# Optimization experiments

Hardware: AMD Instinct MI355X
Metric: run time of the kernel (lower is better)

The kernel has to match this reference:

```python
import jax, jax.numpy as jnp
import numpy as np

DIM = 768
HEADS = 12
HEAD_DIM = DIM // HEADS


def setup_inputs() -> dict:
    key = jax.random.key(0)
    ks = jax.random.split(key, 6)
    B, Nq, Nkv = 2, 2048, 2048
    s = 0.02
    return {
        "query_source": jax.random.normal(ks[0], (B, Nq, DIM), jnp.float32),
        "kv_source": jax.random.normal(ks[1], (B, Nkv, DIM), jnp.float32),
        "Wq": jax.random.normal(ks[2], (DIM, DIM), jnp.float32) * s,
        "Wkv": jax.random.normal(ks[3], (DIM, 2 * DIM), jnp.float32) * s,
        "Wproj": jax.random.normal(ks[4], (DIM, DIM), jnp.float32) * s,
        "bproj": jax.random.normal(ks[5], (DIM,), jnp.float32) * s,
    }


def reference(query_source, kv_source, Wq, Wkv, Wproj, bproj):
    B, Nq, D = query_source.shape
    Nkv = kv_source.shape[1]
    scale = HEAD_DIM ** -0.5
    # projections (qkv_bias=False)
    q = (query_source @ Wq).reshape(B, Nq, HEADS, HEAD_DIM)
    kv = (kv_source @ Wkv).reshape(B, Nkv, 2, HEADS, HEAD_DIM)
    k, v = kv[:, :, 0], kv[:, :, 1]  # (B, Nkv, H, Dh)
    # scores: (B, H, Nq, Nkv)
    attn = jnp.einsum("bqhd,bkhd->bhqk", q, k) * scale
    attn = jax.nn.softmax(attn, axis=-1)
    # attn_drop = 0 (eval)
    x = jnp.einsum("bhqk,bkhd->bqhd", attn, v).reshape(B, Nq, D)
    return x @ Wproj + bproj
```

## Files before the change

### kernel.cpp

```cpp
#include <hip/hip_runtime.h>
#include <math.h>
#include <stdint.h>

typedef __bf16 bf16_t;
typedef __attribute__((ext_vector_type(8))) __bf16 bf16x8;
typedef __attribute__((ext_vector_type(4))) __bf16 bf16x4;
typedef __attribute__((ext_vector_type(4))) float f32x4;

#define DIM   768
#define HEADS 12
#define HD    64
#define NB    2
#define NQ    2048
#define NKV   2048
#define MROWS 4096
#define NQKV  2304

__device__ __forceinline__ float fast_exp2(float x)
{
#if __has_builtin(__builtin_amdgcn_exp2f)
    return __builtin_amdgcn_exp2f(x);
#else
    return exp2f(x);
#endif
}

__device__ __forceinline__ uint32_t pack_bf16x2(float a, float b)
{
    const uint32_t lo = __builtin_bit_cast(uint32_t, a) + 0x8000u;
    const uint32_t hi = __builtin_bit_cast(uint32_t, b) + 0x8000u;
#if __has_builtin(__builtin_amdgcn_perm)
    return __builtin_amdgcn_perm(hi, lo, 0x07060302u);
#else
    return (lo >> 16) | (hi & 0xffff0000u);
#endif
}

__device__ __forceinline__ void async_copy16(const bf16_t* g, bf16_t* l)
{
    typedef const __attribute__((address_space(1))) uint32_t* gp_t;
    typedef __attribute__((address_space(3))) uint32_t* lp_t;
    __builtin_amdgcn_global_load_lds((gp_t)(const void*)g, (lp_t)(void*)l, 16, 0, 0);
}

__global__ void cast2_bf16(const float* __restrict__ a, bf16_t* __restrict__ oa,
                           const float* __restrict__ b, bf16_t* __restrict__ ob, int n)
{
    const float* in  = blockIdx.z ? b : a;
    bf16_t*      out = blockIdx.z ? ob : oa;
    int i = (blockIdx.x * blockDim.x + threadIdx.x) * 8;
    if (i >= n) return;
    bf16x8 v;
#pragma unroll
    for (int j = 0; j < 8; j++) v[j] = (bf16_t)in[i + j];
    *(bf16x8*)(out + i) = v;
}

__global__ void transpose_cast_all(const float* __restrict__ Wq, const float* __restrict__ Wkv,
                                   const float* __restrict__ Wproj, bf16_t* __restrict__ Wt)
{
    const int z = blockIdx.z;
    const float* W; bf16_t* T; int N;
    if (z == 0)      { W = Wq;    T = Wt;                        N = DIM; }
    else if (z == 1) { W = Wkv;   T = Wt + (size_t)DIM * DIM;    N = 2 * DIM; }
    else             { W = Wproj; T = Wt + (size_t)NQKV * DIM;   N = DIM; }
    const int n0 = blockIdx.x * 32;
    if (n0 >= N) return;
    const int k0 = blockIdx.y * 32;
    __shared__ float tile[32][33];
    const int tx = threadIdx.x & 31, ty = threadIdx.x >> 5;
#pragma unroll
    for (int i = 0; i < 4; i++)
        tile[ty + i * 8][tx] = W[(size_t)(k0 + ty + i * 8) * N + n0 + tx];
    __syncthreads();
#pragma unroll
    for (int i = 0; i < 4; i++)
        T[(size_t)(n0 + ty + i * 8) * DIM + k0 + tx] = (bf16_t)tile[tx][ty + i * 8];
}

template<int MODE, int TN>
__global__ __launch_bounds__(256)
void gemm_bk64(const bf16_t* __restrict__ Aq, const bf16_t* __restrict__ Akv,
               const bf16_t* __restrict__ Bt,
               bf16_t* __restrict__ Qb, bf16_t* __restrict__ Kb, bf16_t* __restrict__ Vtb,
               float* __restrict__ ofp, const float* __restrict__ bias, float escale)
{
    constexpr int K  = DIM;
    constexpr int NT = TN / 32;
    constexpr int ABLK = 128 * 64;
    constexpr int BBLK = TN * 64;
    constexpr int SELEMS = (MODE == 0) ? (128 * 136) : (ABLK + BBLK);
    __shared__ __align__(16) bf16_t smem[SELEMS];
    bf16_t* As = smem;
    bf16_t* Bs = smem + ABLK;

    const int tid  = threadIdx.x;
    const int wave = tid >> 6, lane = tid & 63;
    const int quad = lane >> 4, l16 = lane & 15, l7 = l16 & 7;
    const int bm = blockIdx.x * 128, bn = blockIdx.y * TN;
    const int wm = (wave >> 1) * 64, wn = (wave & 1) * (TN / 2);

    const bf16_t* A = (MODE == 0) ? (bn < DIM ? Aq : Akv) : Aq;

    const int srow = tid >> 3;
    const int scol = ((tid & 7) ^ (srow & 7)) * 8;
    const bf16_t* Ag[4];
    const bf16_t* Bg[NT];
#pragma unroll
    for (int i = 0; i < 4; i++)
        Ag[i] = A + (size_t)(bm + i * 32 + srow) * K + scol;
#pragma unroll
    for (int i = 0; i < NT; i++)
        Bg[i] = Bt + (size_t)(bn + i * 32 + srow) * K + scol;
    bf16_t* AsL = As + tid * 8;
    bf16_t* BsL = Bs + tid * 8;

    f32x4 acc[4][NT] = {};

    for (int k0 = 0; k0 < K; k0 += 64) {
#pragma unroll
        for (int i = 0; i < 4; i++) async_copy16(Ag[i] + k0, AsL + i * 2048);
#pragma unroll
        for (int i = 0; i < NT; i++) async_copy16(Bg[i] + k0, BsL + i * 2048);
        __syncthreads();
#pragma unroll
        for (int ks = 0; ks < 2; ks++) {
            const int pc = ((ks * 4 + quad) ^ l7) * 8;
            bf16x8 af[4], bfr[NT];
#pragma unroll
            for (int mt = 0; mt < 4; mt++)
                af[mt] = *(const bf16x8*)(&As[(wm + mt * 16 + l16) * 64 + pc]);
#pragma unroll
            for (int nt = 0; nt < NT; nt++)
                bfr[nt] = *(const bf16x8*)(&Bs[(wn + nt * 16 + l16) * 64 + pc]);
#pragma unroll
            for (int mt = 0; mt < 4; mt++)
#pragma unroll
                for (int nt = 0; nt < NT; nt++)
                    acc[mt][nt] = __builtin_amdgcn_mfma_f32_16x16x32_bf16(
                        af[mt], bfr[nt], acc[mt][nt], 0, 0, 0);
        }
        __syncthreads();
    }

    if (MODE == 1) {
#pragma unroll
        for (int mt = 0; mt < 4; mt++)
#pragma unroll
            for (int nt = 0; nt < NT; nt++)
#pragma unroll
                for (int r = 0; r < 4; r++) {
                    const int gm = bm + wm + mt * 16 + quad * 4 + r;
                    const int gn = bn + wn + nt * 16 + l16;
                    ofp[(size_t)gm * DIM + gn] = acc[mt][nt][r] + bias[gn];
                }
    } else if (bn < DIM) {
#pragma unroll
        for (int mt = 0; mt < 4; mt++)
#pragma unroll
            for (int nt = 0; nt < NT; nt++)
#pragma unroll
                for (int r = 0; r < 4; r++) {
                    const int gm = bm + wm + mt * 16 + quad * 4 + r;
                    const int gn = bn + wn + nt * 16 + l16;
                    Qb[(size_t)gm * DIM + gn] = (bf16_t)(acc[mt][nt][r] * escale);
                }
    } else if (bn < 2 * DIM) {
#pragma unroll
        for (int mt = 0; mt < 4; mt++)
#pragma unroll
            for (int nt = 0; nt < NT; nt++)
#pragma unroll
                for (int r = 0; r < 4; r++) {
                    const int gm = bm + wm + mt * 16 + quad * 4 + r;
                    const int gn = bn + wn + nt * 16 + l16 - DIM;
                    Kb[(size_t)gm * DIM + gn] = (bf16_t)acc[mt][nt][r];
                }
    } else {
        bf16_t* tr = smem;
#pragma unroll
        for (int mt = 0; mt < 4; mt++)
#pragma unroll
            for (int nt = 0; nt < NT; nt++) {
                bf16x4 tv;
#pragma unroll
                for (int r = 0; r < 4; r++) tv[r] = (bf16_t)acc[mt][nt][r];
                *(bf16x4*)(&tr[(wn + nt * 16 + l16) * 136 + wm + mt * 16 + quad * 4]) = tv;
            }
        __syncthreads();
        const int b = bm >> 11, kv0 = bm & 2047;
        const int n2base = bn - 2 * DIM;
        const int cg = tid & 15, cc = cg >> 2, cq = cg & 3;
#pragma unroll
        for (int i = 0; i < 8; i++) {
            const int row = i * 16 + (tid >> 4);
            const int n2 = n2base + row, h = n2 >> 6, d = n2 & 63;
            const bf16x4 lo4 = *(const bf16x4*)(&tr[row * 136 + cc * 32 + cq * 4]);
            const bf16x4 hi4 = *(const bf16x4*)(&tr[row * 136 + cc * 32 + 16 + cq * 4]);
            bf16x8 vv;
#pragma unroll
            for (int j = 0; j < 4; j++) { vv[j] = lo4[j]; vv[4 + j] = hi4[j]; }
            *(bf16x8*)(Vtb + ((size_t)(b * HEADS + h) * HD + d) * NKV + kv0 + cg * 8) = vv;
        }
    }
}

__global__ __launch_bounds__(256, 3)
void attn_kernel(const bf16_t* __restrict__ Qb, const bf16_t* __restrict__ Kb,
                 const bf16_t* __restrict__ Vt, bf16_t* __restrict__ Xb)
{
    __shared__ __align__(16) bf16_t kvbuf[16384];
    __shared__ float libuf[4][2][16];

    const int tid  = threadIdx.x;
    const int wave = tid >> 6, lane = tid & 63;
    const int quad = lane >> 4, l16 = lane & 15;
    const int l7   = l16 & 7;
    const int qh = wave & 1, kvh = wave >> 1;
    const int bh = blockIdx.x;
    const int b = bh / HEADS, h = bh % HEADS;
    const int q0 = blockIdx.y * 64;

    const bf16_t* Qp = Qb + (size_t)b * NQ * DIM + h * HD;
    const bf16_t* Kp = Kb + (size_t)b * NKV * DIM + h * HD;
    const bf16_t* Vp = Vt + (size_t)(b * HEADS + h) * HD * NKV;

    bf16x8 qf[2][2];
#pragma unroll
    for (int qt = 0; qt < 2; qt++)
#pragma unroll
        for (int ks = 0; ks < 2; ks++)
            qf[qt][ks] = *(const bf16x8*)(Qp + (size_t)(q0 + qh * 32 + qt * 16 + l16) * DIM
                                          + ks * 32 + quad * 8);

    const int kl8 = lane >> 3;
    const bf16_t* Kg0 = Kp + (size_t)(wave * 32 + kl8) * DIM + (((lane & 7) ^ kl8) * 8);
    bf16_t* KgL = kvbuf + wave * 2048 + lane * 8;
    const int vl4 = lane >> 4, vp = lane & 15;
    const bf16_t* Vg0[4];
#pragma unroll
    for (int i = 0; i < 4; i++) {
        const int d = wave * 16 + i * 4 + vl4;
        const int c = (vp & 8) | ((vp & 7) ^ (d & 7));
        Vg0[i] = Vp + (size_t)d * NKV + c * 8;
    }
    bf16_t* VgL = kvbuf + 8192 + wave * 2048 + lane * 8;

    f32x4 o[4][2] = {};
    float li[2] = {0.0f, 0.0f};

    for (int t = 0; t < NKV / 128; t++) {
        const int kv0 = t * 128;
#pragma unroll
        for (int i = 0; i < 4; i++)
            async_copy16(Kg0 + (size_t)(kv0 + i * 8) * DIM, KgL + i * 512);
#pragma unroll
        for (int i = 0; i < 4; i++)
            async_copy16(Vg0[i] + kv0, VgL + i * 512);
        __syncthreads();

        f32x4 s[4][2] = {};
#pragma unroll
        for (int kt = 0; kt < 4; kt++)
#pragma unroll
            for (int ks = 0; ks < 2; ks++) {
                const bf16x8 kf = *(const bf16x8*)(&kvbuf[
                    (kvh * 64 + kt * 16 + l16) * 64 + ((((ks << 2) | quad) ^ l7) * 8)]);
#pragma unroll
                for (int qt = 0; qt < 2; qt++)
                    s[kt][qt] = __builtin_amdgcn_mfma_f32_16x16x32_bf16(
                        kf, qf[qt][ks], s[kt][qt], 0, 0, 0);
            }

        bf16x8 pb[2][2];
#pragma unroll
        for (int qt = 0; qt < 2; qt++) {
            float p[16];
#pragma unroll
            for (int kt = 0; kt < 4; kt++)
#pragma unroll
                for (int r = 0; r < 4; r++) p[kt * 4 + r] = fast_exp2(s[kt][qt][r]);
            float rs = 0.0f;
#pragma unroll
            for (int j = 0; j < 16; j++) rs += p[j];
            li[qt] += rs;
#pragma unroll
            for (int kc = 0; kc < 2; kc++) {
                union { uint32_t u[4]; bf16x8 v; } pu;
#pragma unroll
                for (int i = 0; i < 4; i++)
                    pu.u[i] = pack_bf16x2(p[kc * 8 + 2 * i], p[kc * 8 + 2 * i + 1]);
                pb[qt][kc] = pu.v;
            }
        }

#pragma unroll
        for (int dt = 0; dt < 4; dt++) {
            const int droff = 8192 + (dt * 16 + l16) * 128;
#pragma unroll
            for (int kc = 0; kc < 2; kc++) {
                const bf16x8 vf = *(const bf16x8*)(&kvbuf[
                    droff + (kvh * 8 + ((kc * 4 + quad) ^ l7)) * 8]);
#pragma unroll
                for (int qt = 0; qt < 2; qt++)
                    o[dt][qt] = __builtin_amdgcn_mfma_f32_16x16x32_bf16(
                        vf, pb[qt][kc], o[dt][qt], 0, 0, 0);
            }
        }
        __syncthreads();
    }

#pragma unroll
    for (int qt = 0; qt < 2; qt++) {
        li[qt] += __shfl_xor(li[qt], 16);
        li[qt] += __shfl_xor(li[qt], 32);
    }
    if (quad == 0) { libuf[wave][0][l16] = li[0]; libuf[wave][1][l16] = li[1]; }

    float* ob = (float*)(kvbuf + qh * 8192);
    if (kvh == 1) {
#pragma unroll
        for (int dt = 0; dt < 4; dt++)
#pragma unroll
            for (int qt = 0; qt < 2; qt++)
#pragma unroll
                for (int r = 0; r < 4; r++)
                    ob[(dt * 16 + quad * 4 + r) * 33 + qt * 16 + l16] = o[dt][qt][r];
    }
    __syncthreads();
    if (kvh == 0) {
        const float inv0 = 1.0f / (li[0] + libuf[2 + qh][0][l16]);
        const float inv1 = 1.0f / (li[1] + libuf[2 + qh][1][l16]);
#pragma unroll
        for (int dt = 0; dt < 4; dt++)
#pragma unroll
            for (int qt = 0; qt < 2; qt++)
#pragma unroll
                for (int r = 0; r < 4; r++)
                    o[dt][qt][r] = (o[dt][qt][r]
                                    + ob[(dt * 16 + quad * 4 + r) * 33 + qt * 16 + l16])
                                   * (qt ? inv1 : inv0);
    }
    __syncthreads();
    bf16_t* Ob16 = kvbuf;
    if (kvh == 0) {
#pragma unroll
        for (int dt = 0; dt < 4; dt++)
#pragma unroll
            for (int qt = 0; qt < 2; qt++) {
                bf16x4 ov;
#pragma unroll
                for (int r = 0; r < 4; r++) ov[r] = (bf16_t)o[dt][qt][r];
                *(bf16x4*)(&Ob16[(qh * 32 + qt * 16 + l16) * 72 + dt * 16 + quad * 4]) = ov;
            }
    }
    __syncthreads();
    {
        const int row = tid >> 2, ch = (tid & 3) * 16;
        bf16_t* dst = Xb + (size_t)(b * NQ + q0 + row) * DIM + h * HD + ch;
        *(bf16x8*)(dst)     = *(const bf16x8*)(&Ob16[row * 72 + ch]);
        *(bf16x8*)(dst + 8) = *(const bf16x8*)(&Ob16[row * 72 + ch + 8]);
    }
}

extern "C" void kernel_launch(void* const* d_in, const int* in_sizes, int n_in,
                              void* d_out, int out_size, void* d_ws, size_t ws_size,
                              hipStream_t stream)
{
    const float* qs    = (const float*)d_in[0];
    const float* kvs   = (const float*)d_in[1];
    const float* Wq    = (const float*)d_in[2];
    const float* Wkv   = (const float*)d_in[3];
    const float* Wproj = (const float*)d_in[4];
    const float* bproj = (const float*)d_in[5];
    float* out = (float*)d_out;

    bf16_t* w = (bf16_t*)d_ws;
    bf16_t* qs_bf  = w;  w += (size_t)MROWS * DIM;
    bf16_t* kvs_bf = w;  w += (size_t)MROWS * DIM;
    bf16_t* Wt     = w;  w += (size_t)NQKV * DIM;
    bf16_t* Wprojt = w;  w += (size_t)DIM * DIM;
    bf16_t* Qb     = w;  w += (size_t)MROWS * DIM;
    bf16_t* Kb     = w;  w += (size_t)MROWS * DIM;
    bf16_t* Vtb    = w;  w += (size_t)MROWS * DIM;
    bf16_t* Xb     = qs_bf;

    const int n1 = MROWS * DIM;
    cast2_bf16<<<dim3(n1 / 8 / 256, 1, 2), 256, 0, stream>>>(qs, qs_bf, kvs, kvs_bf, n1);
    transpose_cast_all<<<dim3(48, 24, 3), 256, 0, stream>>>(Wq, Wkv, Wproj, Wt);

    const float escale = 0.125f * 1.44269504088896341f;
    gemm_bk64<0, 128><<<dim3(MROWS / 128, NQKV / 128), 256, 0, stream>>>(
        qs_bf, kvs_bf, Wt, Qb, Kb, Vtb, nullptr, nullptr, escale);
    attn_kernel<<<dim3(NB * HEADS, NQ / 64), 256, 0, stream>>>(Qb, Kb, Vtb, Xb);
    gemm_bk64<1, 64><<<dim3(MROWS / 128, DIM / 64), 256, 0, stream>>>(
        Xb, nullptr, Wprojt, nullptr, nullptr, nullptr, out, bproj, 1.0f);
}
```

Baseline: 161.0 us.

## Double-buffer K/V tiles in attention and merge prep kernels into one launch

The attention kernel now double-buffers its K/V LDS tiles. The next tile's async global-to-LDS copies are issued before computing on the current tile, which removes one barrier per iteration and lets loads overlap the MFMA work. The LDS footprint doubles, so occupancy hint drops from 3 to 2 blocks. The two preprocessing kernels (activation cast and weight transpose-cast) are merged into one launch, and the softmax scale is folded into the transposed Wq instead of being applied in the GEMM epilogue. That changes bf16 rounding slightly and launches many idle blocks for the weight slices.

```diff
diff --git a/kernel.cpp b/kernel.cpp
--- a/kernel.cpp
+++ b/kernel.cpp
@@ -43,31 +43,33 @@
     __builtin_amdgcn_global_load_lds((gp_t)(const void*)g, (lp_t)(void*)l, 16, 0, 0);
 }
 
-__global__ void cast2_bf16(const float* __restrict__ a, bf16_t* __restrict__ oa,
-                           const float* __restrict__ b, bf16_t* __restrict__ ob, int n)
-{
-    const float* in  = blockIdx.z ? b : a;
-    bf16_t*      out = blockIdx.z ? ob : oa;
-    int i = (blockIdx.x * blockDim.x + threadIdx.x) * 8;
-    if (i >= n) return;
-    bf16x8 v;
-#pragma unroll
-    for (int j = 0; j < 8; j++) v[j] = (bf16_t)in[i + j];
-    *(bf16x8*)(out + i) = v;
-}
-
-__global__ void transpose_cast_all(const float* __restrict__ Wq, const float* __restrict__ Wkv,
-                                   const float* __restrict__ Wproj, bf16_t* __restrict__ Wt)
-{
+__global__ void prep_kernel(const float* __restrict__ qs, bf16_t* __restrict__ qs_bf,
+                            const float* __restrict__ kvs, bf16_t* __restrict__ kvs_bf,
+                            const float* __restrict__ Wq, const float* __restrict__ Wkv,
+                            const float* __restrict__ Wproj, bf16_t* __restrict__ Wt,
+                            float escale)
+{
+    __shared__ float tile[32][33];
     const int z = blockIdx.z;
-    const float* W; bf16_t* T; int N;
-    if (z == 0)      { W = Wq;    T = Wt;                        N = DIM; }
-    else if (z == 1) { W = Wkv;   T = Wt + (size_t)DIM * DIM;    N = 2 * DIM; }
-    else             { W = Wproj; T = Wt + (size_t)NQKV * DIM;   N = DIM; }
-    const int n0 = blockIdx.x * 32;
-    if (n0 >= N) return;
-    const int k0 = blockIdx.y * 32;
-    __shared__ float tile[32][33];
+    if (z < 2) {
+        const float* in  = z ? kvs : qs;
+        bf16_t*      out = z ? kvs_bf : qs_bf;
+        const int i = (blockIdx.x * 256 + threadIdx.x) * 8;
+        bf16x8 v;
+#pragma unroll
+        for (int j = 0; j < 8; j++) v[j] = (bf16_t)in[i + j];
+        *(bf16x8*)(out + i) = v;
+        return;
+    }
+    const int N   = (z == 3) ? 2 * DIM : DIM;
+    const int nb  = N / 32;
+    const int idx = blockIdx.x;
+    if (idx >= nb * (DIM / 32)) return;
+    const float* W = (z == 2) ? Wq : (z == 3) ? Wkv : Wproj;
+    bf16_t* T = Wt + ((z == 2) ? (size_t)0 : (z == 3) ? (size_t)DIM * DIM
+                                                      : (size_t)NQKV * DIM);
+    const float scl = (z == 2) ? escale : 1.0f;
+    const int n0 = (idx % nb) * 32, k0 = (idx / nb) * 32;
     const int tx = threadIdx.x & 31, ty = threadIdx.x >> 5;
 #pragma unroll
     for (int i = 0; i < 4; i++)
@@ -75,7 +77,7 @@
     __syncthreads();
 #pragma unroll
     for (int i = 0; i < 4; i++)
-        T[(size_t)(n0 + ty + i * 8) * DIM + k0 + tx] = (bf16_t)tile[tx][ty + i * 8];
+        T[(size_t)(n0 + ty + i * 8) * DIM + k0 + tx] = (bf16_t)(tile[tx][ty + i * 8] * scl);
 }
 
 template<int MODE, int TN>
@@ -83,7 +85,7 @@
 void gemm_bk64(const bf16_t* __restrict__ Aq, const bf16_t* __restrict__ Akv,
                const bf16_t* __restrict__ Bt,
                bf16_t* __restrict__ Qb, bf16_t* __restrict__ Kb, bf16_t* __restrict__ Vtb,
-               float* __restrict__ ofp, const float* __restrict__ bias, float escale)
+               float* __restrict__ ofp, const float* __restrict__ bias)
 {
     constexpr int K  = DIM;
     constexpr int NT = TN / 32;
@@ -163,7 +165,7 @@
                 for (int r = 0; r < 4; r++) {
                     const int gm = bm + wm + mt * 16 + quad * 4 + r;
                     const int gn = bn + wn + nt * 16 + l16;
-                    Qb[(size_t)gm * DIM + gn] = (bf16_t)(acc[mt][nt][r] * escale);
+                    Qb[(size_t)gm * DIM + gn] = (bf16_t)acc[mt][nt][r];
                 }
     } else if (bn < 2 * DIM) {
 #pragma unroll
@@ -205,11 +207,11 @@
     }
 }
 
-__global__ __launch_bounds__(256, 3)
+__global__ __launch_bounds__(256, 2)
 void attn_kernel(const bf16_t* __restrict__ Qb, const bf16_t* __restrict__ Kb,
                  const bf16_t* __restrict__ Vt, bf16_t* __restrict__ Xb)
 {
-    __shared__ __align__(16) bf16_t kvbuf[16384];
+    __shared__ __align__(16) bf16_t kvbuf[2][16384];
     __shared__ float libuf[4][2][16];
 
     const int tid  = threadIdx.x;
@@ -235,7 +237,6 @@
 
     const int kl8 = lane >> 3;
     const bf16_t* Kg0 = Kp + (size_t)(wave * 32 + kl8) * DIM + (((lane & 7) ^ kl8) * 8);
-    bf16_t* KgL = kvbuf + wave * 2048 + lane * 8;
     const int vl4 = lane >> 4, vp = lane & 15;
     const bf16_t* Vg0[4];
 #pragma unroll
@@ -244,27 +245,38 @@
         const int c = (vp & 8) | ((vp & 7) ^ (d & 7));
         Vg0[i] = Vp + (size_t)d * NKV + c * 8;
     }
-    bf16_t* VgL = kvbuf + 8192 + wave * 2048 + lane * 8;
 
     f32x4 o[4][2] = {};
     float li[2] = {0.0f, 0.0f};
 
+#pragma unroll
+    for (int i = 0; i < 4; i++)
+        async_copy16(Kg0 + (size_t)(i * 8) * DIM, &kvbuf[0][wave * 2048 + lane * 8 + i * 512]);
+#pragma unroll
+    for (int i = 0; i < 4; i++)
+        async_copy16(Vg0[i], &kvbuf[0][8192 + wave * 2048 + lane * 8 + i * 512]);
+
     for (int t = 0; t < NKV / 128; t++) {
-        const int kv0 = t * 128;
-#pragma unroll
-        for (int i = 0; i < 4; i++)
-            async_copy16(Kg0 + (size_t)(kv0 + i * 8) * DIM, KgL + i * 512);
-#pragma unroll
-        for (int i = 0; i < 4; i++)
-            async_copy16(Vg0[i] + kv0, VgL + i * 512);
         __syncthreads();
+        if (t + 1 < NKV / 128) {
+            const int kv1 = (t + 1) * 128;
+            bf16_t* dst = kvbuf[(t + 1) & 1];
+#pragma unroll
+            for (int i = 0; i < 4; i++)
+                async_copy16(Kg0 + (size_t)(kv1 + i * 8) * DIM,
+                             dst + wave * 2048 + lane * 8 + i * 512);
+#pragma unroll
+            for (int i = 0; i < 4; i++)
+                async_copy16(Vg0[i] + kv1, dst + 8192 + wave * 2048 + lane * 8 + i * 512);
+        }
+        const bf16_t* kb = kvbuf[t & 1];
 
         f32x4 s[4][2] = {};
 #pragma unroll
         for (int kt = 0; kt < 4; kt++)
 #pragma unroll
             for (int ks = 0; ks < 2; ks++) {
-                const bf16x8 kf = *(const bf16x8*)(&kvbuf[
+                const bf16x8 kf = *(const bf16x8*)(&kb[
                     (kvh * 64 + kt * 16 + l16) * 64 + ((((ks << 2) | quad) ^ l7) * 8)]);
 #pragma unroll
                 for (int qt = 0; qt < 2; qt++)
@@ -299,7 +311,7 @@
             const int droff = 8192 + (dt * 16 + l16) * 128;
 #pragma unroll
             for (int kc = 0; kc < 2; kc++) {
-                const bf16x8 vf = *(const bf16x8*)(&kvbuf[
+                const bf16x8 vf = *(const bf16x8*)(&kb[
                     droff + (kvh * 8 + ((kc * 4 + quad) ^ l7)) * 8]);
 #pragma unroll
                 for (int qt = 0; qt < 2; qt++)
@@ -307,7 +319,6 @@
                         vf, pb[qt][kc], o[dt][qt], 0, 0, 0);
             }
         }
-        __syncthreads();
     }
 
 #pragma unroll
@@ -317,7 +328,7 @@
     }
     if (quad == 0) { libuf[wave][0][l16] = li[0]; libuf[wave][1][l16] = li[1]; }
 
-    float* ob = (float*)(kvbuf + qh * 8192);
+    float* ob = (float*)(&kvbuf[0][0] + qh * 8192);
     if (kvh == 1) {
 #pragma unroll
         for (int dt = 0; dt < 4; dt++)
@@ -342,7 +353,7 @@
                                    * (qt ? inv1 : inv0);
     }
     __syncthreads();
-    bf16_t* Ob16 = kvbuf;
+    bf16_t* Ob16 = &kvbuf[0][0];
     if (kvh == 0) {
 #pragma unroll
         for (int dt = 0; dt < 4; dt++)
@@ -385,14 +396,13 @@
     bf16_t* Vtb    = w;  w += (size_t)MROWS * DIM;
     bf16_t* Xb     = qs_bf;
 
-    const int n1 = MROWS * DIM;
-    cast2_bf16<<<dim3(n1 / 8 / 256, 1, 2), 256, 0, stream>>>(qs, qs_bf, kvs, kvs_bf, n1);
-    transpose_cast_all<<<dim3(48, 24, 3), 256, 0, stream>>>(Wq, Wkv, Wproj, Wt);
-
     const float escale = 0.125f * 1.44269504088896341f;
+    prep_kernel<<<dim3(MROWS * DIM / 2048, 1, 5), 256, 0, stream>>>(
+        qs, qs_bf, kvs, kvs_bf, Wq, Wkv, Wproj, Wt, escale);
+
     gemm_bk64<0, 128><<<dim3(MROWS / 128, NQKV / 128), 256, 0, stream>>>(
-        qs_bf, kvs_bf, Wt, Qb, Kb, Vtb, nullptr, nullptr, escale);
+        qs_bf, kvs_bf, Wt, Qb, Kb, Vtb, nullptr, nullptr);
     attn_kernel<<<dim3(NB * HEADS, NQ / 64), 256, 0, stream>>>(Qb, Kb, Vtb, Xb);
     gemm_bk64<1, 64><<<dim3(MROWS / 128, DIM / 64), 256, 0, stream>>>(
-        Xb, nullptr, Wprojt, nullptr, nullptr, nullptr, out, bproj, 1.0f);
-}
+        Xb, nullptr, Wprojt, nullptr, nullptr, nullptr, out, bproj);
+}
```

Result: slower. 171.3 us (+6.4%).
